# Kernel optimization log

Measured on AMD Instinct MI355X. Metric: run time of the kernel, lower is better.

Reference implementation:

```python
import jax, jax.numpy as jnp
import numpy as np

B, N, C, H = 8, 512, 64, 128
T, K = 10, 2                       # dilation threshold and skip divisor
TAUS = (0.25, 0.5, 0.75)
WTS = (0.25, 0.5, 0.25)
EPS_GIN = 0.0                      # (1 + eps) * x, eps buffer
AVG_DEG = 32.0


def setup_inputs() -> dict:
    key = jax.random.key(0)
    ks = jax.random.split(key, 6)
    x = jax.random.normal(ks[0], (B, N, C), jnp.float32)
    u = jax.random.uniform(ks[1], (B, N, N))
    a = u < (AVG_DEG / N)
    adj = jnp.maximum(a, jnp.swapaxes(a, 1, 2)).astype(jnp.float32)  # symmetric binary adjacency
    mask = jax.random.bernoulli(ks[2], 0.9, (B, N))
    W1 = jax.random.normal(ks[3], (C, H), jnp.float32) / np.float32(np.sqrt(C))
    b1 = jnp.zeros((H,), jnp.float32)
    W2 = jax.random.normal(ks[4], (H, C), jnp.float32) / np.float32(np.sqrt(H))
    b2 = jnp.zeros((C,), jnp.float32)
    return {"x": x, "adj": adj, "mask": mask, "W1": W1, "b1": b1, "W2": W2, "b2": b2}


def reference(x, adj, mask, W1, b1, W2, b2):
    Bc, Nc, Cc = x.shape
    eye = jnp.eye(Nc, dtype=bool)
    adj_ = jnp.where(eye, 1.0, adj)                 # add_loop=True: force self loops
    # ---- vectorized dilation (replaces the per-(b,n) python loop) ----
    neigh = (adj_ > 0) & (~eye)                     # neighbors excluding self [B,N,N]
    ni = neigh.astype(jnp.int32)
    rank = jnp.cumsum(ni, axis=-1) - ni             # exclusive rank of m among n's sorted neighbors
    nb = ni.sum(-1)                                 # [B,N] neighbor count (w/o self)
    skip = jnp.where(nb > T, (nb + K - 1) // K, 1)  # ceil(nb/k) if nb > T else 1 (linear mode, layer 1)
    skip = jnp.maximum(skip, 1)
    sk = skip[:, :, None]
    # remove relative indices skip-1, 2*skip-1, ... when skip > 1, only for masked-in nodes
    rem = neigh & (sk > 1) & ((rank % sk) == (sk - 1)) & mask[:, :, None]
    rem = rem | jnp.swapaxes(rem, 1, 2)             # symmetric removal
    adj_d = jnp.where(rem, 0.0, adj_)
    # ---- masked quantile aggregation over neighbors (== nanquantile) ----
    nd = adj_d > 0                                  # includes self loop -> at least 1 valid
    vals = jnp.where(nd[..., None], x[:, None, :, :], jnp.inf)  # [B,N,M,C]; invalid -> +inf
    s = jnp.sort(vals, axis=2)                      # valid values first, ascending
    nv = nd.sum(2)                                  # [B,N] valid count per node
    agg = jnp.zeros_like(x)
    for tau, w in zip(TAUS, WTS):                   # small fixed loop over quantiles
        pos = jnp.asarray(tau, x.dtype) * jnp.maximum(nv - 1, 0).astype(x.dtype)
        lo = jnp.floor(pos).astype(jnp.int32)
        hi = jnp.ceil(pos).astype(jnp.int32)
        frac = (pos - lo.astype(x.dtype))[..., None]
        idx_lo = jnp.broadcast_to(lo[:, :, None, None], (Bc, Nc, 1, Cc))
        idx_hi = jnp.broadcast_to(hi[:, :, None, None], (Bc, Nc, 1, Cc))
        v_lo = jnp.take_along_axis(s, idx_lo, axis=2)[:, :, 0, :]
        v_hi = jnp.take_along_axis(s, idx_hi, axis=2)[:, :, 0, :]
        agg = agg + jnp.asarray(w, x.dtype) * (v_lo + frac * (v_hi - v_lo))
    agg = jnp.where(nv[..., None] > 0, agg, 0.0)    # nan_to_num for empty rows
    out = (1.0 + EPS_GIN) * x + agg
    h = jax.nn.relu(out @ W1 + b1)                  # GIN MLP: Linear-ReLU-Linear
    y = h @ W2 + b2
    return y * mask[..., None].astype(y.dtype)
```

## Files before the change

### kernel.cpp

```cpp
#include <hip/hip_runtime.h>
#include <cstdint>

#define B_ 8
#define N_ 512
#define C_ 64
#define H_ 128
#define T_ 10
#define K_ 2
#define WPR 16
#define NVMAX 96
#define TT 16

__device__ inline uint32_t fkey(float v) {
    uint32_t bits = __float_as_uint(v);
    return (bits & 0x80000000u) ? ~bits : (bits | 0x80000000u);
}
__device__ inline float fdec(uint32_t key) {
    uint32_t ok = (key & 0xFFFFFF00u) | 0x80u;
    uint32_t bits = (ok & 0x80000000u) ? (ok ^ 0x80000000u) : ~ok;
    return __uint_as_float(bits);
}

__global__ __launch_bounds__(256) void pass1_rem(const float* __restrict__ adj,
                                                 const int* __restrict__ mask,
                                                 uint32_t* __restrict__ rembits) {
    int wid = threadIdx.x >> 6, lane = threadIdx.x & 63;
    int row = blockIdx.x * 4 + wid;
    int i = row & (N_ - 1);
    const float4* arow4 = (const float4*)(adj + (size_t)row * N_);
    float4 a0 = arow4[lane * 2];
    float4 a1 = arow4[lane * 2 + 1];
    float av[8] = {a0.x, a0.y, a0.z, a0.w, a1.x, a1.y, a1.z, a1.w};

    int flags = 0, cnt = 0;
    int jbase = lane * 8;
#pragma unroll
    for (int k = 0; k < 8; ++k) {
        int j = jbase + k;
        bool ng = (j != i) && (av[k] > 0.0f);
        flags |= ((int)ng) << k;
        cnt += (int)ng;
    }
    int inc = cnt;
#pragma unroll
    for (int d = 1; d < 64; d <<= 1) {
        int o = __shfl_up(inc, d, 64);
        if (lane >= d) inc += o;
    }
    int excl = inc - cnt;
    int nb = __shfl(inc, 63, 64);
    int skip = (nb > T_) ? ((nb + K_ - 1) / K_) : 1;
    if (skip < 1) skip = 1;
    int maski = mask[row];

    unsigned byteval = 0;
    if (skip > 1 && maski != 0) {
        int r = excl % skip;
#pragma unroll
        for (int k = 0; k < 8; ++k) {
            if ((flags >> k) & 1) {
                if (r == skip - 1) { byteval |= 1u << k; r = 0; }
                else ++r;
            }
        }
    }
    unsigned b0 = __shfl((int)byteval, (lane & 15) * 4 + 0, 64);
    unsigned b1 = __shfl((int)byteval, (lane & 15) * 4 + 1, 64);
    unsigned b2 = __shfl((int)byteval, (lane & 15) * 4 + 2, 64);
    unsigned b3 = __shfl((int)byteval, (lane & 15) * 4 + 3, 64);
    if (lane < WPR) {
        uint32_t w = b0 | (b1 << 8) | (b2 << 16) | (b3 << 24);
        rembits[(size_t)row * WPR + lane] = w;
    }
}

__global__ __launch_bounds__(256) void pass2_quant_mlp(
        const float* __restrict__ x, const float* __restrict__ adj,
        const int* __restrict__ mask, const uint32_t* __restrict__ rembits,
        const float* __restrict__ W1, const float* __restrict__ b1,
        const float* __restrict__ W2, const float* __restrict__ b2,
        float* __restrict__ out) {
    int row = blockIdx.x;
    int b = row >> 9, i = row & (N_ - 1);
    int tid = threadIdx.x;
    int lane = tid & 63;
    int q = tid >> 6;

    __shared__ unsigned short kept[NVMAX];
    __shared__ int s_cnt;
    __shared__ uint32_t keys[NVMAX * C_];
    __shared__ float selv[6][C_];
    __shared__ int s_rr[6];
    __shared__ float s_frac[3];
    __shared__ float out_node[C_];
    __shared__ float hbuf[H_];

    if (tid == 0) s_cnt = 0;
    __syncthreads();

    const float* arow = adj + (size_t)row * N_;
    const uint32_t* rrow = rembits + (size_t)row * WPR;
    const uint32_t* rbase = rembits + (size_t)(b * N_) * WPR;

    for (int jb = 0; jb < N_; jb += 256) {
        int j = jb + tid;
        bool keep;
        if (j == i) {
            keep = true;
        } else {
            keep = (arow[j] > 0.0f);
            if (keep) {
                unsigned rij = (rrow[j >> 5] >> (j & 31)) & 1u;
                unsigned rji = (rbase[(size_t)j * WPR + (i >> 5)] >> (i & 31)) & 1u;
                keep = ((rij | rji) == 0u);
            }
        }
        unsigned long long bal = __ballot(keep);
        int base = 0;
        if (lane == 0 && bal) base = atomicAdd(&s_cnt, __popcll(bal));
        base = __shfl(base, 0, 64);
        if (keep) {
            int pos = __popcll(bal & ((1ull << lane) - 1ull));
            int p = base + pos;
            if (p < NVMAX) kept[p] = (unsigned short)j;
        }
    }
    __syncthreads();
    int nv = s_cnt;
    if (nv > NVMAX) nv = NVMAX;

    const float* xb = x + (size_t)b * N_ * C_;

    for (int t = q; t < nv; t += 4) {
        float v = xb[(size_t)kept[t] * C_ + lane];
        keys[t * C_ + lane] = (fkey(v) & 0xFFFFFF00u) | (uint32_t)t;
    }

    if (tid == 0) {
        const float taus[3] = {0.25f, 0.5f, 0.75f};
        float nm1 = (float)((nv - 1 > 0) ? nv - 1 : 0);
        for (int qq = 0; qq < 3; ++qq) {
            float pos = taus[qq] * nm1;
            int lo = (int)floorf(pos);
            int hi = (int)ceilf(pos);
            s_rr[2 * qq] = lo; s_rr[2 * qq + 1] = hi;
            s_frac[qq] = pos - (float)lo;
        }
    }

    float xself = 0.0f;
    if (q == 0) xself = xb[(size_t)i * C_ + lane];
    __syncthreads();

    int rr0 = s_rr[0], rr1 = s_rr[1], rr2 = s_rr[2],
        rr3 = s_rr[3], rr4 = s_rr[4], rr5 = s_rr[5];

    const uint32_t* kcol = keys + lane;

    for (int base = 0; base < nv; base += 64) {
        int tbase = base + q * TT;
        if (tbase >= nv) continue;
        uint32_t k[TT];
        int rs_a[TT], rs_b[TT];
#pragma unroll
        for (int m = 0; m < TT; ++m) {
            int t = tbase + m;
            k[m] = (t < nv) ? kcol[t * C_] : 0xFFFFFFFFu;
            rs_a[m] = 0; rs_b[m] = 0;
        }
        int u = 0;
#pragma unroll 2
        for (; u + 1 < nv; u += 2) {
            uint32_t w0 = kcol[u * C_];
            uint32_t w1 = kcol[(u + 1) * C_];
#pragma unroll
            for (int m = 0; m < TT; ++m) {
                rs_a[m] += (int)(w0 < k[m]);
                rs_b[m] += (int)(w1 < k[m]);
            }
        }
        if (u < nv) {
            uint32_t w0 = kcol[u * C_];
#pragma unroll
            for (int m = 0; m < TT; ++m) rs_a[m] += (int)(w0 < k[m]);
        }
#pragma unroll
        for (int m = 0; m < TT; ++m) {
            int rs = rs_a[m] + rs_b[m];
            bool h0 = rs == rr0, h1 = rs == rr1, h2 = rs == rr2;
            bool h3 = rs == rr3, h4 = rs == rr4, h5 = rs == rr5;
            if (h0 | h1 | h2 | h3 | h4 | h5) {
                float fv = fdec(k[m]);
                if (h0) selv[0][lane] = fv;
                if (h1) selv[1][lane] = fv;
                if (h2) selv[2][lane] = fv;
                if (h3) selv[3][lane] = fv;
                if (h4) selv[4][lane] = fv;
                if (h5) selv[5][lane] = fv;
            }
        }
    }
    __syncthreads();

    if (tid < C_) {
        float f0 = s_frac[0], f1 = s_frac[1], f2 = s_frac[2];
        float agg = 0.25f * (selv[0][tid] + f0 * (selv[1][tid] - selv[0][tid]));
        agg      += 0.5f  * (selv[2][tid] + f1 * (selv[3][tid] - selv[2][tid]));
        agg      += 0.25f * (selv[4][tid] + f2 * (selv[5][tid] - selv[4][tid]));
        out_node[tid] = xself + agg;
    }
    __syncthreads();

    float maskf = (mask[row] != 0) ? 1.0f : 0.0f;
    {
        int h = tid >> 1, half = tid & 1;
        int c0 = half * 32;
        float acc = 0.0f;
#pragma unroll 4
        for (int c = 0; c < 32; ++c)
            acc += out_node[c0 + c] * W1[(size_t)(c0 + c) * H_ + h];
        acc += __shfl_xor(acc, 1, 64);
        if (half == 0) {
            float v = acc + b1[h];
            hbuf[h] = v > 0.0f ? v : 0.0f;
        }
    }
    __syncthreads();
    {
        int c = tid >> 2, quad = tid & 3;
        int k0 = quad * 32;
        float acc = 0.0f;
#pragma unroll 4
        for (int k = 0; k < 32; ++k)
            acc += hbuf[k0 + k] * W2[(size_t)(k0 + k) * C_ + c];
        acc += __shfl_xor(acc, 1, 64);
        acc += __shfl_xor(acc, 2, 64);
        if (quad == 0)
            out[(size_t)row * C_ + c] = (acc + b2[c]) * maskf;
    }
}

extern "C" void kernel_launch(void* const* d_in, const int* in_sizes, int n_in,
                              void* d_out, int out_size, void* d_ws, size_t ws_size,
                              hipStream_t stream) {
    const float* x   = (const float*)d_in[0];
    const float* adj = (const float*)d_in[1];
    const int*  mask = (const int*)d_in[2];
    const float* W1  = (const float*)d_in[3];
    const float* b1  = (const float*)d_in[4];
    const float* W2  = (const float*)d_in[5];
    const float* b2  = (const float*)d_in[6];
    float* out = (float*)d_out;

    uint32_t* rembits = (uint32_t*)d_ws;

    hipLaunchKernelGGL(pass1_rem, dim3(B_ * N_ / 4), dim3(256), 0, stream,
                       adj, mask, rembits);
    hipLaunchKernelGGL(pass2_quant_mlp, dim3(B_ * N_), dim3(256), 0, stream,
                       x, adj, mask, rembits, W1, b1, W2, b2, out);
}
```

Measured before the change: 182.1 us.

## Rebalance rank-count tiling and coalesce MLP weight loads in quantile kernel

Halves the per-wave candidate tile from 16 to 8 keys and raises the comparison unroll to four accumulators, so that for typical neighbor counts (around 30–40) all four waves get work instead of only the first one or two. It adds a single range check that skips the six-way rank matching for most keys. The two MLP matvecs are remapped so that consecutive lanes read consecutive weight columns, giving coalesced global loads. The second layer reduces across waves through shared memory reused from the key buffer, which costs one extra barrier.

```diff
diff --git a/kernel.cpp b/kernel.cpp
--- a/kernel.cpp
+++ b/kernel.cpp
@@ -9,7 +9,7 @@
 #define K_ 2
 #define WPR 16
 #define NVMAX 96
-#define TT 16
+#define TT 8
 
 __device__ inline uint32_t fkey(float v) {
     uint32_t bits = __float_as_uint(v);
@@ -154,49 +154,55 @@
 
     int rr0 = s_rr[0], rr1 = s_rr[1], rr2 = s_rr[2],
         rr3 = s_rr[3], rr4 = s_rr[4], rr5 = s_rr[5];
+    unsigned rspan = (unsigned)(rr5 - rr0);
 
     const uint32_t* kcol = keys + lane;
 
-    for (int base = 0; base < nv; base += 64) {
+    for (int base = 0; base < nv; base += 32) {
         int tbase = base + q * TT;
         if (tbase >= nv) continue;
         uint32_t k[TT];
-        int rs_a[TT], rs_b[TT];
+        int rs_a[TT], rs_b[TT], rs_c[TT], rs_d[TT];
 #pragma unroll
         for (int m = 0; m < TT; ++m) {
             int t = tbase + m;
             k[m] = (t < nv) ? kcol[t * C_] : 0xFFFFFFFFu;
-            rs_a[m] = 0; rs_b[m] = 0;
+            rs_a[m] = 0; rs_b[m] = 0; rs_c[m] = 0; rs_d[m] = 0;
         }
         int u = 0;
-#pragma unroll 2
-        for (; u + 1 < nv; u += 2) {
-            uint32_t w0 = kcol[u * C_];
+        for (; u + 3 < nv; u += 4) {
+            uint32_t w0 = kcol[(u + 0) * C_];
             uint32_t w1 = kcol[(u + 1) * C_];
+            uint32_t w2 = kcol[(u + 2) * C_];
+            uint32_t w3 = kcol[(u + 3) * C_];
 #pragma unroll
             for (int m = 0; m < TT; ++m) {
                 rs_a[m] += (int)(w0 < k[m]);
                 rs_b[m] += (int)(w1 < k[m]);
-            }
-        }
-        if (u < nv) {
+                rs_c[m] += (int)(w2 < k[m]);
+                rs_d[m] += (int)(w3 < k[m]);
+            }
+        }
+        for (; u < nv; ++u) {
             uint32_t w0 = kcol[u * C_];
 #pragma unroll
             for (int m = 0; m < TT; ++m) rs_a[m] += (int)(w0 < k[m]);
         }
 #pragma unroll
         for (int m = 0; m < TT; ++m) {
-            int rs = rs_a[m] + rs_b[m];
-            bool h0 = rs == rr0, h1 = rs == rr1, h2 = rs == rr2;
-            bool h3 = rs == rr3, h4 = rs == rr4, h5 = rs == rr5;
-            if (h0 | h1 | h2 | h3 | h4 | h5) {
-                float fv = fdec(k[m]);
-                if (h0) selv[0][lane] = fv;
-                if (h1) selv[1][lane] = fv;
-                if (h2) selv[2][lane] = fv;
-                if (h3) selv[3][lane] = fv;
-                if (h4) selv[4][lane] = fv;
-                if (h5) selv[5][lane] = fv;
+            int rs = (rs_a[m] + rs_b[m]) + (rs_c[m] + rs_d[m]);
+            if ((unsigned)(rs - rr0) <= rspan) {
+                bool h0 = rs == rr0, h1 = rs == rr1, h2 = rs == rr2;
+                bool h3 = rs == rr3, h4 = rs == rr4, h5 = rs == rr5;
+                if (h0 | h1 | h2 | h3 | h4 | h5) {
+                    float fv = fdec(k[m]);
+                    if (h0) selv[0][lane] = fv;
+                    if (h1) selv[1][lane] = fv;
+                    if (h2) selv[2][lane] = fv;
+                    if (h3) selv[3][lane] = fv;
+                    if (h4) selv[4][lane] = fv;
+                    if (h5) selv[5][lane] = fv;
+                }
             }
         }
     }
@@ -212,31 +218,40 @@
     __syncthreads();
 
     float maskf = (mask[row] != 0) ? 1.0f : 0.0f;
+
     {
-        int h = tid >> 1, half = tid & 1;
-        int c0 = half * 32;
+        int h = q * 32 + (lane & 31);
+        int kh = (lane >> 5) * 32;
+        int stag = (lane >> 5) * 16;
         float acc = 0.0f;
 #pragma unroll 4
-        for (int c = 0; c < 32; ++c)
-            acc += out_node[c0 + c] * W1[(size_t)(c0 + c) * H_ + h];
-        acc += __shfl_xor(acc, 1, 64);
-        if (half == 0) {
+        for (int c = 0; c < 32; ++c) {
+            int cc = kh + ((c + stag) & 31);
+            acc += out_node[cc] * W1[(size_t)cc * H_ + h];
+        }
+        acc += __shfl_xor(acc, 32, 64);
+        if ((lane >> 5) == 0) {
             float v = acc + b1[h];
             hbuf[h] = v > 0.0f ? v : 0.0f;
         }
     }
     __syncthreads();
+
+    float* part = (float*)keys;
     {
-        int c = tid >> 2, quad = tid & 3;
-        int k0 = quad * 32;
+        int k0 = q * 32;
         float acc = 0.0f;
 #pragma unroll 4
-        for (int k = 0; k < 32; ++k)
-            acc += hbuf[k0 + k] * W2[(size_t)(k0 + k) * C_ + c];
-        acc += __shfl_xor(acc, 1, 64);
-        acc += __shfl_xor(acc, 2, 64);
-        if (quad == 0)
-            out[(size_t)row * C_ + c] = (acc + b2[c]) * maskf;
+        for (int k = 0; k < 32; ++k) {
+            int kk = k0 + k;
+            acc += hbuf[kk] * W2[(size_t)kk * C_ + lane];
+        }
+        part[q * C_ + lane] = acc;
+    }
+    __syncthreads();
+    if (q == 0) {
+        float r = part[lane] + part[C_ + lane] + part[2 * C_ + lane] + part[3 * C_ + lane];
+        out[(size_t)row * C_ + lane] = (r + b2[lane]) * maskf;
     }
 }
 
```

New measurement: 175.3 us. 3.7% less time.
